# Optimization experiments

Hardware: AMD Instinct MI355X
Metric: run time of the kernel (lower is better)

Reference implementation:

```python
import jax, jax.numpy as jnp
import numpy as np

N = 100000
E = 1600000
F_IN = 128
H = 128
NUM_GRAPHS = 512
EPS = 1e-5


def setup_inputs() -> dict:
    key = jax.random.key(0)
    ks = jax.random.split(key, 16)
    x = jax.random.normal(ks[0], (N, F_IN), dtype=jnp.float32)
    edge_index = jax.random.randint(ks[1], (2, E), 0, N, dtype=jnp.int32)
    batch = jnp.sort(jax.random.randint(ks[2], (N,), 0, NUM_GRAPHS, dtype=jnp.int32))
    def lin(k, fi, fo):
        s = 1.0 / np.sqrt(fi)
        return jax.random.uniform(k, (fi, fo), jnp.float32, -s, s)
    return {
        "x": x, "edge_index": edge_index, "batch": batch,
        "W1": lin(ks[3], F_IN, H), "b1": jnp.zeros((H,), jnp.float32),
        "g1": jnp.ones((H,), jnp.float32), "beta1": jnp.zeros((H,), jnp.float32),
        "W2": lin(ks[4], H, H), "b2": jnp.zeros((H,), jnp.float32),
        "g2": jnp.ones((H,), jnp.float32), "beta2": jnp.zeros((H,), jnp.float32),
        "W3": lin(ks[5], H, H), "b3": jnp.zeros((H,), jnp.float32),
        "g3": jnp.ones((H,), jnp.float32), "beta3": jnp.zeros((H,), jnp.float32),
        "Wl": lin(ks[6], H, 1), "bl": jnp.zeros((1,), jnp.float32),
    }


def _layer_norm(x, g, b):
    mu = jnp.mean(x, axis=-1, keepdims=True)
    var = jnp.mean((x - mu) ** 2, axis=-1, keepdims=True)
    return (x - mu) * jax.lax.rsqrt(var + EPS) * g + b


def _gcn_conv(x, W, b, src, dst, dinv):
    # GCNConv: D^{-1/2}(A+I)D^{-1/2} X W + b, deg includes self-loops
    h = x @ W                                   # [N,H]
    enorm = dinv[src] * dinv[dst]               # [E]
    agg = jax.ops.segment_sum(h[src] * enorm[:, None], dst, num_segments=N)
    agg = agg + h * (dinv * dinv)[:, None]      # self-loop contribution
    return agg + b


def reference(x, edge_index, batch, W1, b1, g1, beta1, W2, b2, g2, beta2,
              W3, b3, g3, beta3, Wl, bl):
    src, dst = edge_index[0], edge_index[1]
    deg = 1.0 + jax.ops.segment_sum(jnp.ones((E,), jnp.float32), dst, num_segments=N)
    dinv = jax.lax.rsqrt(deg)
    h = jax.nn.relu(_layer_norm(_gcn_conv(x, W1, b1, src, dst, dinv), g1, beta1))
    h = jax.nn.relu(_layer_norm(_gcn_conv(h, W2, b2, src, dst, dinv), g2, beta2))
    h = jax.nn.relu(_layer_norm(_gcn_conv(h, W3, b3, src, dst, dinv), g3, beta3))
    # global mean pool over graphs
    sums = jax.ops.segment_sum(h, batch, num_segments=NUM_GRAPHS)
    cnts = jax.ops.segment_sum(jnp.ones((N,), jnp.float32), batch, num_segments=NUM_GRAPHS)
    pooled = sums / jnp.maximum(cnts, 1.0)[:, None]
    return pooled @ Wl + bl                     # [NUM_GRAPHS, 1]
```

## Files before the change

### kernel.cpp

```cpp
#include <hip/hip_runtime.h>
#include <hip/hip_bf16.h>
#include <math.h>

#define N_NODES    100000
#define N_EDGES    1600000
#define FDIM       128
#define NUM_GRAPHS 512
#define EPS        1e-5f
#define PADN       100096

#define B_CVT   12512
#define B_WPK   192

#define NBUCK   196
#define CAPA    9216
#define EB_CHUNK 2048
#define BIN_BLOCKS ((N_EDGES + EB_CHUNK - 1) / EB_CHUNK)
#define SEGSH   14
#define SEGN    8

typedef __attribute__((ext_vector_type(8))) __bf16 bf16x8;
typedef __attribute__((ext_vector_type(4))) float  f32x4;

__device__ __forceinline__ unsigned short f2bf(float f) {
    unsigned u = __builtin_bit_cast(unsigned, f);
    u += 0x7FFF + ((u >> 16) & 1);
    return (unsigned short)(u >> 16);
}
__device__ __forceinline__ float bf2f(unsigned short b) {
    unsigned u = ((unsigned)b) << 16;
    return __builtin_bit_cast(float, u);
}

__device__ __forceinline__ void dec4(unsigned dw, float* o) {
    auto lo = __builtin_amdgcn_cvt_pk_f32_fp8(dw, false);
    auto hi = __builtin_amdgcn_cvt_pk_f32_fp8(dw, true);
    o[0] = lo[0]; o[1] = lo[1]; o[2] = hi[0]; o[3] = hi[1];
}

__device__ __forceinline__ void acc16(uint4 v, float* a) {
    float d[16];
    dec4(v.x, &d[0]); dec4(v.y, &d[4]); dec4(v.z, &d[8]); dec4(v.w, &d[12]);
#pragma unroll
    for (int f = 0; f < 16; f++) a[f] += d[f];
}


__global__ __launch_bounds__(256) void k_bin(const int* __restrict__ src,
                                             const int* __restrict__ dst,
                                             int* __restrict__ bcur,
                                             unsigned* __restrict__ binned) {
    __shared__ int hist[NBUCK];
    __shared__ int lbase[NBUCK];
    __shared__ int loff[NBUCK];
    __shared__ unsigned lpack[EB_CHUNK];
    __shared__ unsigned short lbuck[EB_CHUNK];
    int b = blockIdx.x;
    int t = threadIdx.x;
    int e0 = b * EB_CHUNK;
    int nE = min(EB_CHUNK, N_EDGES - e0);

    for (int j = t; j < NBUCK; j += 256) { hist[j] = 0; loff[j] = 0; }
    __syncthreads();

    for (int k = t; k < nE; k += 256) {
        int e  = e0 + k;
        int d  = dst[e];
        int bk = d >> 9;
        lpack[k] = (unsigned)src[e] | ((unsigned)(d & 511) << 17);
        lbuck[k] = (unsigned short)bk;
        atomicAdd(&hist[bk], 1);
    }
    __syncthreads();
    for (int j = t; j < NBUCK; j += 256)
        lbase[j] = atomicAdd(&bcur[j], hist[j]);
    __syncthreads();

    for (int k = t; k < nE; k += 256) {
        int bk = lbuck[k];
        int p  = lbase[bk] + atomicAdd(&loff[bk], 1);
        binned[(size_t)bk * CAPA + p] = lpack[k];
    }
}


__global__ __launch_bounds__(256) void k_mid(const unsigned* __restrict__ binned,
                                             const int* __restrict__ bcur,
                                             int* __restrict__ offs,
                                             float* __restrict__ dinv,
                                             int* __restrict__ csr_src,
                                             const float* __restrict__ x,
                                             unsigned short* __restrict__ xb,
                                             const float* __restrict__ W1,
                                             const float* __restrict__ W2,
                                             const float* __restrict__ W3,
                                             unsigned short* __restrict__ wp) {
    __shared__ int smem[512 * SEGN + 256 + CAPA];
    int b = blockIdx.x;
    int t = threadIdx.x;

    if (b < NBUCK) {
        int* cnt2  = smem;
        int* part  = smem + 4096;
        int* stage = smem + 4352;
        int nb0 = b * 512;
        int cnt = bcur[b];

        int pv = (t < b) ? bcur[t] : 0;
#pragma unroll
        for (int off = 32; off; off >>= 1) pv += __shfl_down(pv, off);
        if ((t & 63) == 0) part[t >> 6] = pv;
        __syncthreads();
        int seg0 = part[0] + part[1] + part[2] + part[3];
        __syncthreads();

        for (int j = t; j < 512 * SEGN; j += 256) cnt2[j] = 0;
        __syncthreads();

        for (int k = t; k < cnt; k += 256) {
            unsigned v = binned[(size_t)b * CAPA + k];
            atomicAdd(&cnt2[(v >> 17) * SEGN + ((v & 0x1FFFF) >> SEGSH)], 1);
        }
        __syncthreads();

        int base16 = t * 16;
        int lsum[16];
        int run = 0;
#pragma unroll
        for (int q = 0; q < 16; q++) { lsum[q] = run; run += cnt2[base16 + q]; }
        int deg0 = lsum[8];
        int deg1 = run - lsum[8];
        part[t] = run;
        __syncthreads();
        for (int off = 1; off < 256; off <<= 1) {
            int y = 0;
            if (t >= off) y = part[t - off];
            __syncthreads();
            if (t >= off) part[t] += y;
            __syncthreads();
        }
        int excl = part[t] - run;
#pragma unroll
        for (int q = 0; q < 16; q++) cnt2[base16 + q] = excl + lsum[q];

        {
            int n0 = nb0 + 2 * t;
            if (n0 < N_NODES) {
                offs[n0] = seg0 + excl;
                dinv[n0] = rsqrtf(1.0f + (float)deg0);
            }
            if (n0 + 1 < N_NODES) {
                offs[n0 + 1] = seg0 + excl + lsum[8];
                dinv[n0 + 1] = rsqrtf(1.0f + (float)deg1);
            }
        }
        if (b == NBUCK - 1 && t == 0) offs[N_NODES] = N_EDGES;
        __syncthreads();

        for (int k = t; k < cnt; k += 256) {
            unsigned v = binned[(size_t)b * CAPA + k];
            int p = atomicAdd(&cnt2[(v >> 17) * SEGN + ((v & 0x1FFFF) >> SEGSH)], 1);
            stage[p] = (int)(v & 0x1FFFF);
        }
        __syncthreads();
        for (int k = t; k < cnt; k += 256) csr_src[seg0 + k] = stage[k];
    } else if (b < NBUCK + B_CVT) {
        long long idx = ((long long)(b - NBUCK) * 256 + t) * 4;
        ushort4 o;
        if (idx < (long long)N_NODES * FDIM) {
            float4 v = *(const float4*)(x + idx);
            o.x = f2bf(v.x); o.y = f2bf(v.y); o.z = f2bf(v.z); o.w = f2bf(v.w);
        } else {
            o.x = o.y = o.z = o.w = 0;
        }
        *(ushort4*)(xb + idx) = o;
    } else {
        int wb  = b - (NBUCK + B_CVT);
        int mat = wb >> 6;
        const float* W = (mat == 0) ? W1 : (mat == 1) ? W2 : W3;
        unsigned short* o = wp + (size_t)mat * 16384;
        int idx = (wb & 63) * 256 + t;
        int j  = idx & 7;
        int l  = (idx >> 3) & 63;
        int ct = (idx >> 9) & 7;
        int ks = idx >> 12;
        int k  = ks * 32 + (l >> 4) * 8 + j;
        int c  = ct * 16 + (l & 15);
        o[idx] = f2bf(W[k * 128 + c]);
    }
}


__global__ __launch_bounds__(256) void k_gemm(const unsigned short* __restrict__ A,
                                              const unsigned short* __restrict__ Wp,
                                              const float* __restrict__ dinv,
                                              unsigned char* __restrict__ C8) {
    int t    = threadIdx.x;
    int lane = t & 63;
    int w    = t >> 6;
    int wc   = w & 1;
    int wr   = w >> 1;
    int rb   = blockIdx.x * 128 + wr * 64 + (lane & 15);
    int koff = (lane >> 4) * 8;

    f32x4 acc[4][4];
#pragma unroll
    for (int c = 0; c < 4; c++)
#pragma unroll
        for (int r = 0; r < 4; r++) acc[c][r] = (f32x4){0.f, 0.f, 0.f, 0.f};

    const bf16x8* Wv = (const bf16x8*)Wp;
#pragma unroll
    for (int ks = 0; ks < 4; ++ks) {
        bf16x8 fw[4], fa[4];
#pragma unroll
        for (int c = 0; c < 4; ++c)
            fw[c] = Wv[(ks * 8 + wc * 4 + c) * 64 + lane];
#pragma unroll
        for (int r = 0; r < 4; ++r) {
            const uint4 v = *(const uint4*)(A + (size_t)(rb + r * 16) * 128 + ks * 32 + koff);
            fa[r] = __builtin_bit_cast(bf16x8, v);
        }
#pragma unroll
        for (int c = 0; c < 4; ++c)
#pragma unroll
            for (int r = 0; r < 4; ++r)
                acc[c][r] = __builtin_amdgcn_mfma_f32_16x16x32_bf16(fw[c], fa[r], acc[c][r], 0, 0, 0);
    }

#pragma unroll
    for (int r = 0; r < 4; ++r) {
        int row = blockIdx.x * 128 + wr * 64 + r * 16 + (lane & 15);
        if (row < N_NODES) {
            float dv = dinv[row];
#pragma unroll
            for (int c = 0; c < 4; ++c) {
                int col = (wc * 4 + c) * 16 + (lane >> 4) * 4;
                unsigned u = __builtin_amdgcn_cvt_pk_fp8_f32(acc[c][r][0] * dv, acc[c][r][1] * dv, 0, false);
                u = (unsigned)__builtin_amdgcn_cvt_pk_fp8_f32(acc[c][r][2] * dv, acc[c][r][3] * dv, (int)u, true);
                *(unsigned*)(C8 + (size_t)row * 128 + col) = u;
            }
        }
    }
}


__global__ __launch_bounds__(256) void k_agg(const unsigned char* __restrict__ h8,
                                             unsigned short* __restrict__ out,
                                             const int* __restrict__ offs,
                                             const int* __restrict__ csr_src,
                                             const float* __restrict__ dinv,
                                             const float* __restrict__ bias,
                                             const float* __restrict__ gamma,
                                             const float* __restrict__ beta) {
    int t    = threadIdx.x;
    int lane = t & 63;
    int grp  = lane >> 3;
    int sl   = lane & 7;
    int i    = blockIdx.x * 32 + (t >> 6) * 8 + grp;

    float di = dinv[i];
    size_t lofs16 = (size_t)sl * 16;

    float a[16];
    {
        uint4 v = *(const uint4*)(h8 + (size_t)i * 128 + lofs16);
        float d[16];
        dec4(v.x, &d[0]); dec4(v.y, &d[4]); dec4(v.z, &d[8]); dec4(v.w, &d[12]);
#pragma unroll
        for (int f = 0; f < 16; f++) a[f] = d[f];
    }

    int eBeg = offs[i], eEnd = offs[i + 1];
    int e = eBeg;
    int s0, s1, s2, s3;
    if (e + 4 <= eEnd) {
        s0 = csr_src[e + 0]; s1 = csr_src[e + 1];
        s2 = csr_src[e + 2]; s3 = csr_src[e + 3];
    }
    for (; e + 8 <= eEnd; e += 4) {
        uint4 v0 = *(const uint4*)(h8 + (size_t)s0 * 128 + lofs16);
        uint4 v1 = *(const uint4*)(h8 + (size_t)s1 * 128 + lofs16);
        uint4 v2 = *(const uint4*)(h8 + (size_t)s2 * 128 + lofs16);
        uint4 v3 = *(const uint4*)(h8 + (size_t)s3 * 128 + lofs16);
        s0 = csr_src[e + 4]; s1 = csr_src[e + 5];
        s2 = csr_src[e + 6]; s3 = csr_src[e + 7];
        acc16(v0, a); acc16(v1, a); acc16(v2, a); acc16(v3, a);
    }
    if (e + 4 <= eEnd) {
        uint4 v0 = *(const uint4*)(h8 + (size_t)s0 * 128 + lofs16);
        uint4 v1 = *(const uint4*)(h8 + (size_t)s1 * 128 + lofs16);
        uint4 v2 = *(const uint4*)(h8 + (size_t)s2 * 128 + lofs16);
        uint4 v3 = *(const uint4*)(h8 + (size_t)s3 * 128 + lofs16);
        acc16(v0, a); acc16(v1, a); acc16(v2, a); acc16(v3, a);
        e += 4;
    }
    for (; e < eEnd; ++e) {
        int s = csr_src[e];
        uint4 v = *(const uint4*)(h8 + (size_t)s * 128 + lofs16);
        acc16(v, a);
    }

    float4 b0 = *(const float4*)(bias + sl * 16);
    float4 b1 = *(const float4*)(bias + sl * 16 + 4);
    float4 b2 = *(const float4*)(bias + sl * 16 + 8);
    float4 b3 = *(const float4*)(bias + sl * 16 + 12);
    a[0]  = fmaf(a[0],  di, b0.x); a[1]  = fmaf(a[1],  di, b0.y);
    a[2]  = fmaf(a[2],  di, b0.z); a[3]  = fmaf(a[3],  di, b0.w);
    a[4]  = fmaf(a[4],  di, b1.x); a[5]  = fmaf(a[5],  di, b1.y);
    a[6]  = fmaf(a[6],  di, b1.z); a[7]  = fmaf(a[7],  di, b1.w);
    a[8]  = fmaf(a[8],  di, b2.x); a[9]  = fmaf(a[9],  di, b2.y);
    a[10] = fmaf(a[10], di, b2.z); a[11] = fmaf(a[11], di, b2.w);
    a[12] = fmaf(a[12], di, b3.x); a[13] = fmaf(a[13], di, b3.y);
    a[14] = fmaf(a[14], di, b3.z); a[15] = fmaf(a[15], di, b3.w);

    float s1v = 0.f, s2v = 0.f;
#pragma unroll
    for (int f = 0; f < 16; f++) { s1v += a[f]; s2v += a[f] * a[f]; }
#pragma unroll
    for (int off = 1; off < 8; off <<= 1) {
        s1v += __shfl_xor(s1v, off);
        s2v += __shfl_xor(s2v, off);
    }
    float mu   = s1v * (1.0f / 128.0f);
    float var  = s2v * (1.0f / 128.0f) - mu * mu;
    float rstd = rsqrtf(var + EPS);

    float g[16], be[16];
    {
        float4 g0 = *(const float4*)(gamma + sl * 16);
        float4 g1 = *(const float4*)(gamma + sl * 16 + 4);
        float4 g2 = *(const float4*)(gamma + sl * 16 + 8);
        float4 g3 = *(const float4*)(gamma + sl * 16 + 12);
        g[0]=g0.x; g[1]=g0.y; g[2]=g0.z; g[3]=g0.w;
        g[4]=g1.x; g[5]=g1.y; g[6]=g1.z; g[7]=g1.w;
        g[8]=g2.x; g[9]=g2.y; g[10]=g2.z; g[11]=g2.w;
        g[12]=g3.x; g[13]=g3.y; g[14]=g3.z; g[15]=g3.w;
        float4 e0v = *(const float4*)(beta + sl * 16);
        float4 e1v = *(const float4*)(beta + sl * 16 + 4);
        float4 e2v = *(const float4*)(beta + sl * 16 + 8);
        float4 e3v = *(const float4*)(beta + sl * 16 + 12);
        be[0]=e0v.x; be[1]=e0v.y; be[2]=e0v.z; be[3]=e0v.w;
        be[4]=e1v.x; be[5]=e1v.y; be[6]=e1v.z; be[7]=e1v.w;
        be[8]=e2v.x; be[9]=e2v.y; be[10]=e2v.z; be[11]=e2v.w;
        be[12]=e3v.x; be[13]=e3v.y; be[14]=e3v.z; be[15]=e3v.w;
    }

    unsigned ow[8];
#pragma unroll
    for (int f = 0; f < 8; f++) {
        float r0 = fmaxf((a[2*f]   - mu) * rstd * g[2*f]   + be[2*f],   0.f);
        float r1 = fmaxf((a[2*f+1] - mu) * rstd * g[2*f+1] + be[2*f+1], 0.f);
        ow[f] = (unsigned)f2bf(r0) | ((unsigned)f2bf(r1) << 16);
    }
    uint4* op = (uint4*)(out + (size_t)i * 128 + sl * 16);
    op[0] = make_uint4(ow[0], ow[1], ow[2], ow[3]);
    op[1] = make_uint4(ow[4], ow[5], ow[6], ow[7]);
}


__global__ __launch_bounds__(256) void k_pool(const unsigned short* __restrict__ h,
                                              const int* __restrict__ batch,
                                              const float* __restrict__ Wl,
                                              const float* __restrict__ bl,
                                              float* __restrict__ out) {
    __shared__ float2 part[4][64];
    int g = blockIdx.x;
    int t = threadIdx.x, w = t >> 6, lane = t & 63;

    int lo = 0, hi = N_NODES;
    while (lo < hi) { int mid = (lo + hi) >> 1; if (batch[mid] < g) lo = mid + 1; else hi = mid; }
    int s = lo;
    lo = s; hi = N_NODES;
    while (lo < hi) { int mid = (lo + hi) >> 1; if (batch[mid] < g + 1) lo = mid + 1; else hi = mid; }
    int e = lo;

    float ax = 0.f, ay = 0.f;
    for (int n = s + w; n < e; n += 4) {
        unsigned v = *(const unsigned*)(h + (size_t)n * 128 + lane * 2);
        ax += bf2f((unsigned short)(v & 0xffff));
        ay += bf2f((unsigned short)(v >> 16));
    }
    part[w][lane] = make_float2(ax, ay);
    __syncthreads();
    if (t < 64) {
        float sx = part[0][lane].x + part[1][lane].x + part[2][lane].x + part[3][lane].x;
        float sy = part[0][lane].y + part[1][lane].y + part[2][lane].y + part[3][lane].y;
        float cnt = fmaxf((float)(e - s), 1.0f);
        float inv = 1.0f / cnt;
        float p = sx * inv * Wl[lane * 2] + sy * inv * Wl[lane * 2 + 1];
#pragma unroll
        for (int off = 32; off; off >>= 1) p += __shfl_xor(p, off);
        if (lane == 0) out[g] = p + bl[0];
    }
}


extern "C" void kernel_launch(void* const* d_in, const int* in_sizes, int n_in,
                              void* d_out, int out_size, void* d_ws, size_t ws_size,
                              hipStream_t stream) {
    const float* x     = (const float*)d_in[0];
    const int*   ei    = (const int*)d_in[1];
    const int*   batch = (const int*)d_in[2];
    const float* W1 = (const float*)d_in[3];
    const float* b1 = (const float*)d_in[4];
    const float* g1 = (const float*)d_in[5];
    const float* be1 = (const float*)d_in[6];
    const float* W2 = (const float*)d_in[7];
    const float* b2 = (const float*)d_in[8];
    const float* g2 = (const float*)d_in[9];
    const float* be2 = (const float*)d_in[10];
    const float* W3 = (const float*)d_in[11];
    const float* b3 = (const float*)d_in[12];
    const float* g3 = (const float*)d_in[13];
    const float* be3 = (const float*)d_in[14];
    const float* Wl = (const float*)d_in[15];
    const float* bl = (const float*)d_in[16];

    const int* src = ei;
    const int* dst = ei + N_EDGES;

    char* ws = (char*)d_ws;
    size_t off = 0;
    auto alloc = [&](size_t bytes) -> void* {
        void* p = ws + off;
        off += (bytes + 255) & ~(size_t)255;
        return p;
    };
    unsigned short* xb   = (unsigned short*)alloc((size_t)PADN * FDIM * 2);
    unsigned short* hA   = (unsigned short*)alloc((size_t)PADN * FDIM * 2);
    unsigned char*  hF   = (unsigned char*)alloc((size_t)PADN * FDIM);
    unsigned short* wp   = (unsigned short*)alloc((size_t)3 * 16384 * 2);
    float* dinv    = (float*)alloc((size_t)N_NODES * 4);
    int*   offs    = (int*)alloc((size_t)(N_NODES + 1) * 4);
    int*   csr_src = (int*)alloc((size_t)N_EDGES * 4);
    unsigned* binned = (unsigned*)alloc((size_t)NBUCK * CAPA * 4);
    int*   bcur    = (int*)alloc(256 * 4);

    hipMemsetAsync(bcur, 0, 256 * 4, stream);

    k_bin<<<BIN_BLOCKS, 256, 0, stream>>>(src, dst, bcur, binned);
    k_mid<<<NBUCK + B_CVT + B_WPK, 256, 0, stream>>>(binned, bcur, offs, dinv, csr_src,
                                                     x, xb, W1, W2, W3, wp);

    int gemm_grid = PADN / 128;
    int agg_grid  = N_NODES / 32;

    k_gemm<<<gemm_grid, 256, 0, stream>>>(xb, wp, dinv, hF);
    k_agg<<<agg_grid, 256, 0, stream>>>(hF, hA, offs, csr_src, dinv, b1, g1, be1);
    k_gemm<<<gemm_grid, 256, 0, stream>>>(hA, wp + 16384, dinv, hF);
    k_agg<<<agg_grid, 256, 0, stream>>>(hF, hA, offs, csr_src, dinv, b2, g2, be2);
    k_gemm<<<gemm_grid, 256, 0, stream>>>(hA, wp + 32768, dinv, hF);
    k_agg<<<agg_grid, 256, 0, stream>>>(hF, hA, offs, csr_src, dinv, b3, g3, be3);

    k_pool<<<NUM_GRAPHS, 256, 0, stream>>>(hA, batch, Wl, bl, (float*)d_out);
}
```

Baseline: 265.4 us.

## Fuse aggregation+layernorm with next layer's GEMM via LDS tile; drop CSR staging

Adds a k_fused kernel that aggregates and layer-normalizes 128 nodes into an LDS bf16 tile, then runs the next layer's MFMA GEMM straight from shared memory. This removes the bf16 hA round trip through global memory and two launches per middle layer, using ping-pong fp8 buffers. The CSR build also scatters directly to global memory instead of staging in LDS. The cost is fewer blocks (782 vs 3125) in the fused kernel, which lowers the parallelism available to hide gather latency.

Result: faster. 244.2 us (-8.0%).

```diff
diff --git a/kernel.cpp b/kernel.cpp
--- a/kernel.cpp
+++ b/kernel.cpp
@@ -43,6 +43,100 @@
     dec4(v.x, &d[0]); dec4(v.y, &d[4]); dec4(v.z, &d[8]); dec4(v.w, &d[12]);
 #pragma unroll
     for (int f = 0; f < 16; f++) a[f] += d[f];
+}
+
+__device__ __forceinline__ void agg_core(const unsigned char* __restrict__ h8,
+                                         const int* __restrict__ offs,
+                                         const int* __restrict__ csr_src,
+                                         float di, int i, int sl,
+                                         const float* __restrict__ bias,
+                                         const float* __restrict__ gamma,
+                                         const float* __restrict__ beta,
+                                         unsigned* ow) {
+    size_t lofs16 = (size_t)sl * 16;
+    float a[16];
+    {
+        uint4 v = *(const uint4*)(h8 + (size_t)i * 128 + lofs16);
+        float d[16];
+        dec4(v.x, &d[0]); dec4(v.y, &d[4]); dec4(v.z, &d[8]); dec4(v.w, &d[12]);
+#pragma unroll
+        for (int f = 0; f < 16; f++) a[f] = d[f];
+    }
+
+    int eBeg = offs[i], eEnd = offs[i + 1];
+    int e = eBeg;
+    int s0, s1, s2, s3;
+    if (e + 4 <= eEnd) {
+        s0 = csr_src[e + 0]; s1 = csr_src[e + 1];
+        s2 = csr_src[e + 2]; s3 = csr_src[e + 3];
+    }
+    for (; e + 8 <= eEnd; e += 4) {
+        uint4 v0 = *(const uint4*)(h8 + (size_t)s0 * 128 + lofs16);
+        uint4 v1 = *(const uint4*)(h8 + (size_t)s1 * 128 + lofs16);
+        uint4 v2 = *(const uint4*)(h8 + (size_t)s2 * 128 + lofs16);
+        uint4 v3 = *(const uint4*)(h8 + (size_t)s3 * 128 + lofs16);
+        s0 = csr_src[e + 4]; s1 = csr_src[e + 5];
+        s2 = csr_src[e + 6]; s3 = csr_src[e + 7];
+        acc16(v0, a); acc16(v1, a); acc16(v2, a); acc16(v3, a);
+    }
+    if (e + 4 <= eEnd) {
+        uint4 v0 = *(const uint4*)(h8 + (size_t)s0 * 128 + lofs16);
+        uint4 v1 = *(const uint4*)(h8 + (size_t)s1 * 128 + lofs16);
+        uint4 v2 = *(const uint4*)(h8 + (size_t)s2 * 128 + lofs16);
+        uint4 v3 = *(const uint4*)(h8 + (size_t)s3 * 128 + lofs16);
+        acc16(v0, a); acc16(v1, a); acc16(v2, a); acc16(v3, a);
+        e += 4;
+    }
+    for (; e < eEnd; ++e) {
+        int s = csr_src[e];
+        uint4 v = *(const uint4*)(h8 + (size_t)s * 128 + lofs16);
+        acc16(v, a);
+    }
+
+    float4 b0 = *(const float4*)(bias + sl * 16);
+    float4 b1 = *(const float4*)(bias + sl * 16 + 4);
+    float4 b2 = *(const float4*)(bias + sl * 16 + 8);
+    float4 b3 = *(const float4*)(bias + sl * 16 + 12);
+    a[0]  = fmaf(a[0],  di, b0.x); a[1]  = fmaf(a[1],  di, b0.y);
+    a[2]  = fmaf(a[2],  di, b0.z); a[3]  = fmaf(a[3],  di, b0.w);
+    a[4]  = fmaf(a[4],  di, b1.x); a[5]  = fmaf(a[5],  di, b1.y);
+    a[6]  = fmaf(a[6],  di, b1.z); a[7]  = fmaf(a[7],  di, b1.w);
+    a[8]  = fmaf(a[8],  di, b2.x); a[9]  = fmaf(a[9],  di, b2.y);
+    a[10] = fmaf(a[10], di, b2.z); a[11] = fmaf(a[11], di, b2.w);
+    a[12] = fmaf(a[12], di, b3.x); a[13] = fmaf(a[13], di, b3.y);
+    a[14] = fmaf(a[14], di, b3.z); a[15] = fmaf(a[15], di, b3.w);
+
+    float s1v = 0.f, s2v = 0.f;
+#pragma unroll
+    for (int f = 0; f < 16; f++) { s1v += a[f]; s2v += a[f] * a[f]; }
+#pragma unroll
+    for (int off = 1; off < 8; off <<= 1) {
+        s1v += __shfl_xor(s1v, off);
+        s2v += __shfl_xor(s2v, off);
+    }
+    float mu   = s1v * (1.0f / 128.0f);
+    float var  = s2v * (1.0f / 128.0f) - mu * mu;
+    float rstd = rsqrtf(var + EPS);
+
+    float4 g0 = *(const float4*)(gamma + sl * 16);
+    float4 g1 = *(const float4*)(gamma + sl * 16 + 4);
+    float4 g2 = *(const float4*)(gamma + sl * 16 + 8);
+    float4 g3 = *(const float4*)(gamma + sl * 16 + 12);
+    float4 e0v = *(const float4*)(beta + sl * 16);
+    float4 e1v = *(const float4*)(beta + sl * 16 + 4);
+    float4 e2v = *(const float4*)(beta + sl * 16 + 8);
+    float4 e3v = *(const float4*)(beta + sl * 16 + 12);
+    float g[16]  = {g0.x,g0.y,g0.z,g0.w, g1.x,g1.y,g1.z,g1.w,
+                    g2.x,g2.y,g2.z,g2.w, g3.x,g3.y,g3.z,g3.w};
+    float be[16] = {e0v.x,e0v.y,e0v.z,e0v.w, e1v.x,e1v.y,e1v.z,e1v.w,
+                    e2v.x,e2v.y,e2v.z,e2v.w, e3v.x,e3v.y,e3v.z,e3v.w};
+
+#pragma unroll
+    for (int f = 0; f < 8; f++) {
+        float r0 = fmaxf((a[2*f]   - mu) * rstd * g[2*f]   + be[2*f],   0.f);
+        float r1 = fmaxf((a[2*f+1] - mu) * rstd * g[2*f+1] + be[2*f+1], 0.f);
+        ow[f] = (unsigned)f2bf(r0) | ((unsigned)f2bf(r1) << 16);
+    }
 }
 
 
@@ -95,14 +189,13 @@
                                              const float* __restrict__ W2,
                                              const float* __restrict__ W3,
                                              unsigned short* __restrict__ wp) {
-    __shared__ int smem[512 * SEGN + 256 + CAPA];
+    __shared__ int smem[512 * SEGN + 256];
     int b = blockIdx.x;
     int t = threadIdx.x;
 
     if (b < NBUCK) {
-        int* cnt2  = smem;
-        int* part  = smem + 4096;
-        int* stage = smem + 4352;
+        int* cnt2 = smem;
+        int* part = smem + 4096;
         int nb0 = b * 512;
         int cnt = bcur[b];
 
@@ -160,10 +253,8 @@
         for (int k = t; k < cnt; k += 256) {
             unsigned v = binned[(size_t)b * CAPA + k];
             int p = atomicAdd(&cnt2[(v >> 17) * SEGN + ((v & 0x1FFFF) >> SEGSH)], 1);
-            stage[p] = (int)(v & 0x1FFFF);
-        }
-        __syncthreads();
-        for (int k = t; k < cnt; k += 256) csr_src[seg0 + k] = stage[k];
+            csr_src[seg0 + p] = (int)(v & 0x1FFFF);
+        }
     } else if (b < NBUCK + B_CVT) {
         long long idx = ((long long)(b - NBUCK) * 256 + t) * 4;
         ushort4 o;
@@ -245,6 +336,89 @@
 }
 
 
+__global__ __launch_bounds__(256, 4) void k_fused(const unsigned char* __restrict__ h8_in,
+                                                  const unsigned short* __restrict__ Wp,
+                                                  const float* __restrict__ dinv,
+                                                  unsigned char* __restrict__ h8_out,
+                                                  const int* __restrict__ offs,
+                                                  const int* __restrict__ csr_src,
+                                                  const float* __restrict__ bias,
+                                                  const float* __restrict__ gamma,
+                                                  const float* __restrict__ beta) {
+    __shared__ unsigned tile_u[128 * 64];
+    int t    = threadIdx.x;
+    int lane = t & 63;
+    int w    = t >> 6;
+    int grp  = lane >> 3;
+    int sl   = lane & 7;
+    int r0   = blockIdx.x * 128;
+
+    for (int pass = 0; pass < 4; ++pass) {
+        int nt = pass * 32 + w * 8 + grp;
+        int i  = r0 + nt;
+        unsigned ow[8];
+        if (i < N_NODES) {
+            agg_core(h8_in, offs, csr_src, dinv[i], i, sl, bias, gamma, beta, ow);
+        } else {
+#pragma unroll
+            for (int f = 0; f < 8; f++) ow[f] = 0;
+        }
+        int rowbase = nt * 64;
+        int colu    = sl * 8;
+        int swz0 = (colu    ) ^ ((nt & 15) << 2);
+        int swz1 = (colu + 4) ^ ((nt & 15) << 2);
+        *(uint4*)&tile_u[rowbase + swz0] = make_uint4(ow[0], ow[1], ow[2], ow[3]);
+        *(uint4*)&tile_u[rowbase + swz1] = make_uint4(ow[4], ow[5], ow[6], ow[7]);
+    }
+    __syncthreads();
+
+    int wc = w & 1;
+    int wr = w >> 1;
+    f32x4 acc[4][4];
+#pragma unroll
+    for (int c = 0; c < 4; c++)
+#pragma unroll
+        for (int r = 0; r < 4; r++) acc[c][r] = (f32x4){0.f, 0.f, 0.f, 0.f};
+
+    const bf16x8* Wv = (const bf16x8*)Wp;
+#pragma unroll
+    for (int ks = 0; ks < 4; ++ks) {
+        bf16x8 fw[4], fa[4];
+#pragma unroll
+        for (int c = 0; c < 4; ++c)
+            fw[c] = Wv[(ks * 8 + wc * 4 + c) * 64 + lane];
+#pragma unroll
+        for (int r = 0; r < 4; ++r) {
+            int lr   = wr * 64 + r * 16 + (lane & 15);
+            int colu = ks * 16 + (lane >> 4) * 4;
+            int swz  = colu ^ ((lr & 15) << 2);
+            uint4 v = *(const uint4*)&tile_u[lr * 64 + swz];
+            fa[r] = __builtin_bit_cast(bf16x8, v);
+        }
+#pragma unroll
+        for (int c = 0; c < 4; ++c)
+#pragma unroll
+            for (int r = 0; r < 4; ++r)
+                acc[c][r] = __builtin_amdgcn_mfma_f32_16x16x32_bf16(fw[c], fa[r], acc[c][r], 0, 0, 0);
+    }
+
+#pragma unroll
+    for (int r = 0; r < 4; ++r) {
+        int row = r0 + wr * 64 + r * 16 + (lane & 15);
+        if (row < N_NODES) {
+            float dv = dinv[row];
+#pragma unroll
+            for (int c = 0; c < 4; ++c) {
+                int col = (wc * 4 + c) * 16 + (lane >> 4) * 4;
+                unsigned u = __builtin_amdgcn_cvt_pk_fp8_f32(acc[c][r][0] * dv, acc[c][r][1] * dv, 0, false);
+                u = (unsigned)__builtin_amdgcn_cvt_pk_fp8_f32(acc[c][r][2] * dv, acc[c][r][3] * dv, (int)u, true);
+                *(unsigned*)(h8_out + (size_t)row * 128 + col) = u;
+            }
+        }
+    }
+}
+
+
 __global__ __launch_bounds__(256) void k_agg(const unsigned char* __restrict__ h8,
                                              unsigned short* __restrict__ out,
                                              const int* __restrict__ offs,
@@ -259,100 +433,9 @@
     int sl   = lane & 7;
     int i    = blockIdx.x * 32 + (t >> 6) * 8 + grp;
 
-    float di = dinv[i];
-    size_t lofs16 = (size_t)sl * 16;
-
-    float a[16];
-    {
-        uint4 v = *(const uint4*)(h8 + (size_t)i * 128 + lofs16);
-        float d[16];
-        dec4(v.x, &d[0]); dec4(v.y, &d[4]); dec4(v.z, &d[8]); dec4(v.w, &d[12]);
-#pragma unroll
-        for (int f = 0; f < 16; f++) a[f] = d[f];
-    }
-
-    int eBeg = offs[i], eEnd = offs[i + 1];
-    int e = eBeg;
-    int s0, s1, s2, s3;
-    if (e + 4 <= eEnd) {
-        s0 = csr_src[e + 0]; s1 = csr_src[e + 1];
-        s2 = csr_src[e + 2]; s3 = csr_src[e + 3];
-    }
-    for (; e + 8 <= eEnd; e += 4) {
-        uint4 v0 = *(const uint4*)(h8 + (size_t)s0 * 128 + lofs16);
-        uint4 v1 = *(const uint4*)(h8 + (size_t)s1 * 128 + lofs16);
-        uint4 v2 = *(const uint4*)(h8 + (size_t)s2 * 128 + lofs16);
-        uint4 v3 = *(const uint4*)(h8 + (size_t)s3 * 128 + lofs16);
-        s0 = csr_src[e + 4]; s1 = csr_src[e + 5];
-        s2 = csr_src[e + 6]; s3 = csr_src[e + 7];
-        acc16(v0, a); acc16(v1, a); acc16(v2, a); acc16(v3, a);
-    }
-    if (e + 4 <= eEnd) {
-        uint4 v0 = *(const uint4*)(h8 + (size_t)s0 * 128 + lofs16);
-        uint4 v1 = *(const uint4*)(h8 + (size_t)s1 * 128 + lofs16);
-        uint4 v2 = *(const uint4*)(h8 + (size_t)s2 * 128 + lofs16);
-        uint4 v3 = *(const uint4*)(h8 + (size_t)s3 * 128 + lofs16);
-        acc16(v0, a); acc16(v1, a); acc16(v2, a); acc16(v3, a);
-        e += 4;
-    }
-    for (; e < eEnd; ++e) {
-        int s = csr_src[e];
-        uint4 v = *(const uint4*)(h8 + (size_t)s * 128 + lofs16);
-        acc16(v, a);
-    }
-
-    float4 b0 = *(const float4*)(bias + sl * 16);
-    float4 b1 = *(const float4*)(bias + sl * 16 + 4);
-    float4 b2 = *(const float4*)(bias + sl * 16 + 8);
-    float4 b3 = *(const float4*)(bias + sl * 16 + 12);
-    a[0]  = fmaf(a[0],  di, b0.x); a[1]  = fmaf(a[1],  di, b0.y);
-    a[2]  = fmaf(a[2],  di, b0.z); a[3]  = fmaf(a[3],  di, b0.w);
-    a[4]  = fmaf(a[4],  di, b1.x); a[5]  = fmaf(a[5],  di, b1.y);
-    a[6]  = fmaf(a[6],  di, b1.z); a[7]  = fmaf(a[7],  di, b1.w);
-    a[8]  = fmaf(a[8],  di, b2.x); a[9]  = fmaf(a[9],  di, b2.y);
-    a[10] = fmaf(a[10], di, b2.z); a[11] = fmaf(a[11], di, b2.w);
-    a[12] = fmaf(a[12], di, b3.x); a[13] = fmaf(a[13], di, b3.y);
-    a[14] = fmaf(a[14], di, b3.z); a[15] = fmaf(a[15], di, b3.w);
-
-    float s1v = 0.f, s2v = 0.f;
-#pragma unroll
-    for (int f = 0; f < 16; f++) { s1v += a[f]; s2v += a[f] * a[f]; }
-#pragma unroll
-    for (int off = 1; off < 8; off <<= 1) {
-        s1v += __shfl_xor(s1v, off);
-        s2v += __shfl_xor(s2v, off);
-    }
-    float mu   = s1v * (1.0f / 128.0f);
-    float var  = s2v * (1.0f / 128.0f) - mu * mu;
-    float rstd = rsqrtf(var + EPS);
-
-    float g[16], be[16];
-    {
-        float4 g0 = *(const float4*)(gamma + sl * 16);
-        float4 g1 = *(const float4*)(gamma + sl * 16 + 4);
-        float4 g2 = *(const float4*)(gamma + sl * 16 + 8);
-        float4 g3 = *(const float4*)(gamma + sl * 16 + 12);
-        g[0]=g0.x; g[1]=g0.y; g[2]=g0.z; g[3]=g0.w;
-        g[4]=g1.x; g[5]=g1.y; g[6]=g1.z; g[7]=g1.w;
-        g[8]=g2.x; g[9]=g2.y; g[10]=g2.z; g[11]=g2.w;
-        g[12]=g3.x; g[13]=g3.y; g[14]=g3.z; g[15]=g3.w;
-        float4 e0v = *(const float4*)(beta + sl * 16);
-        float4 e1v = *(const float4*)(beta + sl * 16 + 4);
-        float4 e2v = *(const float4*)(beta + sl * 16 + 8);
-        float4 e3v = *(const float4*)(beta + sl * 16 + 12);
-        be[0]=e0v.x; be[1]=e0v.y; be[2]=e0v.z; be[3]=e0v.w;
-        be[4]=e1v.x; be[5]=e1v.y; be[6]=e1v.z; be[7]=e1v.w;
-        be[8]=e2v.x; be[9]=e2v.y; be[10]=e2v.z; be[11]=e2v.w;
-        be[12]=e3v.x; be[13]=e3v.y; be[14]=e3v.z; be[15]=e3v.w;
-    }
-
     unsigned ow[8];
-#pragma unroll
-    for (int f = 0; f < 8; f++) {
-        float r0 = fmaxf((a[2*f]   - mu) * rstd * g[2*f]   + be[2*f],   0.f);
-        float r1 = fmaxf((a[2*f+1] - mu) * rstd * g[2*f+1] + be[2*f+1], 0.f);
-        ow[f] = (unsigned)f2bf(r0) | ((unsigned)f2bf(r1) << 16);
-    }
+    agg_core(h8, offs, csr_src, dinv[i], i, sl, bias, gamma, beta, ow);
+
     uint4* op = (uint4*)(out + (size_t)i * 128 + sl * 16);
     op[0] = make_uint4(ow[0], ow[1], ow[2], ow[3]);
     op[1] = make_uint4(ow[4], ow[5], ow[6], ow[7]);
@@ -429,7 +512,8 @@
     };
     unsigned short* xb   = (unsigned short*)alloc((size_t)PADN * FDIM * 2);
     unsigned short* hA   = (unsigned short*)alloc((size_t)PADN * FDIM * 2);
-    unsigned char*  hF   = (unsigned char*)alloc((size_t)PADN * FDIM);
+    unsigned char*  hFa  = (unsigned char*)alloc((size_t)PADN * FDIM);
+    unsigned char*  hFb  = (unsigned char*)alloc((size_t)PADN * FDIM);
     unsigned short* wp   = (unsigned short*)alloc((size_t)3 * 16384 * 2);
     float* dinv    = (float*)alloc((size_t)N_NODES * 4);
     int*   offs    = (int*)alloc((size_t)(N_NODES + 1) * 4);
@@ -443,15 +527,15 @@
     k_mid<<<NBUCK + B_CVT + B_WPK, 256, 0, stream>>>(binned, bcur, offs, dinv, csr_src,
                                                      x, xb, W1, W2, W3, wp);
 
-    int gemm_grid = PADN / 128;
-    int agg_grid  = N_NODES / 32;
-
-    k_gemm<<<gemm_grid, 256, 0, stream>>>(xb, wp, dinv, hF);
-    k_agg<<<agg_grid, 256, 0, stream>>>(hF, hA, offs, csr_src, dinv, b1, g1, be1);
-    k_gemm<<<gemm_grid, 256, 0, stream>>>(hA, wp + 16384, dinv, hF);
-    k_agg<<<agg_grid, 256, 0, stream>>>(hF, hA, offs, csr_src, dinv, b2, g2, be2);
-    k_gemm<<<gemm_grid, 256, 0, stream>>>(hA, wp + 32768, dinv, hF);
-    k_agg<<<agg_grid, 256, 0, stream>>>(hF, hA, offs, csr_src, dinv, b3, g3, be3);
+    int gemm_grid  = PADN / 128;
+    int agg_grid   = N_NODES / 32;
+
+    k_gemm<<<gemm_grid, 256, 0, stream>>>(xb, wp, dinv, hFa);
+    k_fused<<<gemm_grid, 256, 0, stream>>>(hFa, wp + 16384, dinv, hFb,
+                                           offs, csr_src, b1, g1, be1);
+    k_fused<<<gemm_grid, 256, 0, stream>>>(hFb, wp + 32768, dinv, hFa,
+                                           offs, csr_src, b2, g2, be2);
+    k_agg<<<agg_grid, 256, 0, stream>>>(hFa, hA, offs, csr_src, dinv, b3, g3, be3);
 
     k_pool<<<NUM_GRAPHS, 256, 0, stream>>>(hA, batch, Wl, bl, (float*)d_out);
 }
```
